# Kernel optimization log

Hardware: AMD Instinct MI355X
Metric: run time of the kernel (lower is better)

The kernel has to match this reference:

```python
import jax, jax.numpy as jnp
import numpy as np

N = 1_000_000      # occupied voxels
GRID = 256         # voxel grid extent per axis
K = 27             # 3^3 kernel offsets
CIN, COUT = 2, 16


def _build_nbr_map(coords: np.ndarray) -> np.ndarray:
    """Kernel-offset neighbor map like MinkowskiEngine's kernel map.
    coords: [N,3] unique int voxel coords. Returns [N,K] int32, -1 = no neighbor.
    """
    key = (coords[:, 0] * GRID + coords[:, 1]) * GRID + coords[:, 2]
    order = np.argsort(key)
    skey = key[order]
    offsets = np.array([[dx, dy, dz]
                        for dx in (-1, 0, 1)
                        for dy in (-1, 0, 1)
                        for dz in (-1, 0, 1)], dtype=np.int64)
    nbr = np.full((coords.shape[0], K), -1, dtype=np.int32)
    for k in range(K):
        nc = coords + offsets[k]
        valid = np.all((nc >= 0) & (nc < GRID), axis=1)
        nkey = (nc[:, 0] * GRID + nc[:, 1]) * GRID + nc[:, 2]
        pos = np.clip(np.searchsorted(skey, nkey), 0, coords.shape[0] - 1)
        hit = valid & (skey[pos] == nkey)
        nbr[:, k] = np.where(hit, order[pos].astype(np.int32), -1)
    return nbr


def setup_inputs() -> dict:
    rng = np.random.default_rng(0)
    lin = rng.choice(GRID ** 3, size=N, replace=False)  # unique voxel ids
    coords = np.stack([lin // (GRID * GRID), (lin // GRID) % GRID, lin % GRID],
                      axis=1).astype(np.int64)
    nbr = _build_nbr_map(coords)
    key = jax.random.key(0)
    k1, k2 = jax.random.split(key)
    features = jax.random.normal(k1, (N, CIN), dtype=jnp.float32)
    # MinkowskiConvolution kernel: one [Cin,Cout] matrix per kernel offset, no bias
    kernel = jax.random.normal(k2, (K, CIN, COUT), dtype=jnp.float32) * 0.1
    return {"features": features, "kernel": kernel, "nbr_idx": jnp.asarray(nbr)}


def reference(features, kernel, nbr_idx):
    # gather-GEMM-scatter sparse conv: out[n] = sum_k W_k^T x[nbr(n,k)]
    mask = (nbr_idx >= 0)
    safe = jnp.maximum(nbr_idx, 0)
    gathered = features[safe]                              # [N,K,Cin]
    gathered = gathered * mask[..., None].astype(features.dtype)
    return jnp.einsum('nkc,kcd->nd', gathered, kernel)     # [N,Cout]
```

## Files before the change

### kernel.cpp

```cpp
#include <hip/hip_runtime.h>

#define K_OFF 27
#define CIN   2
#define COUT  16
#define BLK   256
#define WPB   4
#define IPW   (64 * K_OFF)
#define NB    8

typedef __attribute__((address_space(3))) unsigned int lds_u32;
typedef __attribute__((address_space(1))) const unsigned int g_u32;

__global__ __launch_bounds__(BLK, 5) void spconv_kernel(
    const float* __restrict__ feats,
    const float* __restrict__ w,
    const int*   __restrict__ nbr,
    float*       __restrict__ out,
    int n_pts)
{
    __shared__ int    s_idx[WPB * IPW];
    __shared__ float4 s_w[8 * K_OFF];

    const int t    = threadIdx.x;
    const int lane = t & 63;
    const int wv   = t >> 6;
    const int tile = blockIdx.x * WPB + wv;
    const int p    = tile * 64 + lane;

    if (t < 8 * K_OFF) {
        const int k = t >> 3, q = t & 7;
        s_w[q * K_OFF + k] = reinterpret_cast<const float4*>(w)[t];
    }

    const bool full = ((tile + 1) * 64 <= n_pts);
    if (full) {
        const int* src = nbr + (size_t)tile * IPW;
        int*       dst = s_idx + wv * IPW;
        #pragma unroll
        for (int j = 0; j < 6; ++j) {
            __builtin_amdgcn_global_load_lds(
                (g_u32*)(src + j * 256 + lane * 4),
                (lds_u32*)(dst + j * 256), 16, 0, 0);
        }
        if (lane < 48) {
            __builtin_amdgcn_global_load_lds(
                (g_u32*)(src + 6 * 256 + lane * 4),
                (lds_u32*)(dst + 6 * 256), 16, 0, 0);
        }
    }
    __syncthreads();

    float acc[COUT];
    #pragma unroll
    for (int d = 0; d < COUT; ++d) acc[d] = 0.f;

    const float2* feats2 = reinterpret_cast<const float2*>(feats);
    const int* rowp = s_idx + wv * IPW + lane * K_OFF;

    unsigned bm = 0;
    if (full) {
        #pragma unroll
        for (int k = 0; k < K_OFF; ++k)
            bm |= (rowp[k] >= 0) ? (1u << k) : 0u;
    }

    int mx = __popc(bm);
    #pragma unroll
    for (int off = 32; off; off >>= 1) mx = max(mx, __shfl_xor(mx, off, 64));

    for (int j0 = 0; j0 < mx; j0 += NB) {
        int  kk[NB];
        bool al[NB];
        #pragma unroll
        for (int j = 0; j < NB; ++j) {
            al[j] = (bm != 0);
            kk[j] = al[j] ? (int)__builtin_ctz(bm) : 0;
            bm &= bm - 1;
        }
        int idx[NB];
        #pragma unroll
        for (int j = 0; j < NB; ++j) idx[j] = rowp[kk[j]];
        float2 f[NB];
        #pragma unroll
        for (int j = 0; j < NB; ++j) f[j] = feats2[al[j] && idx[j] > 0 ? idx[j] : 0];
        #pragma unroll
        for (int j = 0; j < NB; ++j) {
            const float fm = al[j] ? 1.0f : 0.0f;
            const float fx = f[j].x * fm, fy = f[j].y * fm;
            const int k = kk[j];
            #pragma unroll
            for (int q = 0; q < 4; ++q) {
                const float4 wa = s_w[q * K_OFF + k];
                const float4 wb = s_w[(q + 4) * K_OFF + k];
                acc[q*4+0] = fmaf(fy, wb.x, fmaf(fx, wa.x, acc[q*4+0]));
                acc[q*4+1] = fmaf(fy, wb.y, fmaf(fx, wa.y, acc[q*4+1]));
                acc[q*4+2] = fmaf(fy, wb.z, fmaf(fx, wa.z, acc[q*4+2]));
                acc[q*4+3] = fmaf(fy, wb.w, fmaf(fx, wa.w, acc[q*4+3]));
            }
        }
    }

    if (!full) {
        const bool pv = (p < n_pts);
        for (int k = 0; k < K_OFF; ++k) {
            const int idx = pv ? nbr[(size_t)p * K_OFF + k] : -1;
            const float fm = (idx >= 0) ? 1.0f : 0.0f;
            const float2 f = feats2[idx > 0 ? idx : 0];
            const float fx = f.x * fm, fy = f.y * fm;
            #pragma unroll
            for (int q = 0; q < 4; ++q) {
                const float4 wa = s_w[q * K_OFF + k];
                const float4 wb = s_w[(q + 4) * K_OFF + k];
                acc[q*4+0] = fmaf(fy, wb.x, fmaf(fx, wa.x, acc[q*4+0]));
                acc[q*4+1] = fmaf(fy, wb.y, fmaf(fx, wa.y, acc[q*4+1]));
                acc[q*4+2] = fmaf(fy, wb.z, fmaf(fx, wa.z, acc[q*4+2]));
                acc[q*4+3] = fmaf(fy, wb.w, fmaf(fx, wa.w, acc[q*4+3]));
            }
        }
    }

    if (p < n_pts) {
        float4* o = reinterpret_cast<float4*>(out + (size_t)p * COUT);
        o[0] = make_float4(acc[0],  acc[1],  acc[2],  acc[3]);
        o[1] = make_float4(acc[4],  acc[5],  acc[6],  acc[7]);
        o[2] = make_float4(acc[8],  acc[9],  acc[10], acc[11]);
        o[3] = make_float4(acc[12], acc[13], acc[14], acc[15]);
    }
}

extern "C" void kernel_launch(void* const* d_in, const int* in_sizes, int n_in,
                              void* d_out, int out_size, void* d_ws, size_t ws_size,
                              hipStream_t stream) {
    const float* feats = (const float*)d_in[0];
    const float* w     = (const float*)d_in[1];
    const int*   nbr   = (const int*)d_in[2];
    float*       out   = (float*)d_out;

    const int n_pts   = in_sizes[0] / CIN;
    const int n_tiles = (n_pts + 63) / 64;
    const int grid    = (n_tiles + WPB - 1) / WPB;

    spconv_kernel<<<grid, BLK, 0, stream>>>(feats, w, nbr, out, n_pts);
}
```

Baseline: 59.27 us.

## Make kernel persistent with double-buffered async neighbor-index staging

Turns the one-tile-per-wave kernel into a persistent grid-stride loop capped at 512 blocks. Each wave prefetches the next tile's neighbor indices into a second LDS buffer with global_load_lds while it computes the current tile. The aim is to hide index-load latency and drop per-block launch and setup overhead. In exchange, LDS use per block doubles and launch bounds drop to 2 blocks per CU, which reduces occupancy available for hiding the feature-gather latency; the gather batch also shrinks from 8 to 6.

```diff
diff --git a/kernel.cpp b/kernel.cpp
--- a/kernel.cpp
+++ b/kernel.cpp
@@ -6,125 +6,144 @@
 #define BLK   256
 #define WPB   4
 #define IPW   (64 * K_OFF)
-#define NB    8
+#define NB    6
 
 typedef __attribute__((address_space(3))) unsigned int lds_u32;
 typedef __attribute__((address_space(1))) const unsigned int g_u32;
 
-__global__ __launch_bounds__(BLK, 5) void spconv_kernel(
+__device__ __forceinline__ void stage_tile(const int* __restrict__ nbr,
+                                           int tile, int* dst, int lane) {
+    const int* src = nbr + (size_t)tile * IPW;
+    #pragma unroll
+    for (int j = 0; j < 6; ++j)
+        __builtin_amdgcn_global_load_lds((g_u32*)(src + j * 256 + lane * 4),
+                                         (lds_u32*)(dst + j * 256), 16, 0, 0);
+    if (lane < 48)
+        __builtin_amdgcn_global_load_lds((g_u32*)(src + 6 * 256 + lane * 4),
+                                         (lds_u32*)(dst + 6 * 256), 16, 0, 0);
+}
+
+__global__ __launch_bounds__(BLK, 2) void spconv_kernel(
     const float* __restrict__ feats,
     const float* __restrict__ w,
     const int*   __restrict__ nbr,
     float*       __restrict__ out,
-    int n_pts)
+    int n_pts, int n_tiles)
 {
-    __shared__ int    s_idx[WPB * IPW];
+    __shared__ int    s_idx[WPB * 2 * IPW];
     __shared__ float4 s_w[8 * K_OFF];
 
     const int t    = threadIdx.x;
     const int lane = t & 63;
     const int wv   = t >> 6;
-    const int tile = blockIdx.x * WPB + wv;
-    const int p    = tile * 64 + lane;
 
     if (t < 8 * K_OFF) {
         const int k = t >> 3, q = t & 7;
         s_w[q * K_OFF + k] = reinterpret_cast<const float4*>(w)[t];
     }
-
-    const bool full = ((tile + 1) * 64 <= n_pts);
-    if (full) {
-        const int* src = nbr + (size_t)tile * IPW;
-        int*       dst = s_idx + wv * IPW;
-        #pragma unroll
-        for (int j = 0; j < 6; ++j) {
-            __builtin_amdgcn_global_load_lds(
-                (g_u32*)(src + j * 256 + lane * 4),
-                (lds_u32*)(dst + j * 256), 16, 0, 0);
-        }
-        if (lane < 48) {
-            __builtin_amdgcn_global_load_lds(
-                (g_u32*)(src + 6 * 256 + lane * 4),
-                (lds_u32*)(dst + 6 * 256), 16, 0, 0);
-        }
-    }
     __syncthreads();
 
-    float acc[COUT];
-    #pragma unroll
-    for (int d = 0; d < COUT; ++d) acc[d] = 0.f;
+    const int n_waves = gridDim.x * WPB;
+    int* bufA = s_idx + wv * (2 * IPW);
+    int* bufB = bufA + IPW;
 
     const float2* feats2 = reinterpret_cast<const float2*>(feats);
-    const int* rowp = s_idx + wv * IPW + lane * K_OFF;
 
-    unsigned bm = 0;
-    if (full) {
+    int tile = blockIdx.x * WPB + wv;
+    if (tile >= n_tiles) return;
+
+    if ((tile + 1) * 64 <= n_pts) stage_tile(nbr, tile, bufA, lane);
+    int cur = 0;
+
+    while (true) {
+        asm volatile("s_waitcnt vmcnt(0)" ::: "memory");
+        __builtin_amdgcn_sched_barrier(0);
+        __builtin_amdgcn_wave_barrier();
+
+        const int nxt = tile + n_waves;
+        if (nxt < n_tiles && (nxt + 1) * 64 <= n_pts)
+            stage_tile(nbr, nxt, cur ? bufA : bufB, lane);
+
+        int* buf = cur ? bufB : bufA;
+        const bool tfull = ((tile + 1) * 64 <= n_pts);
+
+        float acc[COUT];
         #pragma unroll
-        for (int k = 0; k < K_OFF; ++k)
-            bm |= (rowp[k] >= 0) ? (1u << k) : 0u;
-    }
+        for (int d = 0; d < COUT; ++d) acc[d] = 0.f;
 
-    int mx = __popc(bm);
-    #pragma unroll
-    for (int off = 32; off; off >>= 1) mx = max(mx, __shfl_xor(mx, off, 64));
+        if (tfull) {
+            const int* rowp = buf + lane * K_OFF;
+            unsigned bm = 0;
+            #pragma unroll
+            for (int k = 0; k < K_OFF; ++k)
+                bm |= (rowp[k] >= 0) ? (1u << k) : 0u;
+            int mx = __popc(bm);
+            #pragma unroll
+            for (int off = 32; off; off >>= 1) mx = max(mx, __shfl_xor(mx, off, 64));
 
-    for (int j0 = 0; j0 < mx; j0 += NB) {
-        int  kk[NB];
-        bool al[NB];
-        #pragma unroll
-        for (int j = 0; j < NB; ++j) {
-            al[j] = (bm != 0);
-            kk[j] = al[j] ? (int)__builtin_ctz(bm) : 0;
-            bm &= bm - 1;
-        }
-        int idx[NB];
-        #pragma unroll
-        for (int j = 0; j < NB; ++j) idx[j] = rowp[kk[j]];
-        float2 f[NB];
-        #pragma unroll
-        for (int j = 0; j < NB; ++j) f[j] = feats2[al[j] && idx[j] > 0 ? idx[j] : 0];
-        #pragma unroll
-        for (int j = 0; j < NB; ++j) {
-            const float fm = al[j] ? 1.0f : 0.0f;
-            const float fx = f[j].x * fm, fy = f[j].y * fm;
-            const int k = kk[j];
-            #pragma unroll
-            for (int q = 0; q < 4; ++q) {
-                const float4 wa = s_w[q * K_OFF + k];
-                const float4 wb = s_w[(q + 4) * K_OFF + k];
-                acc[q*4+0] = fmaf(fy, wb.x, fmaf(fx, wa.x, acc[q*4+0]));
-                acc[q*4+1] = fmaf(fy, wb.y, fmaf(fx, wa.y, acc[q*4+1]));
-                acc[q*4+2] = fmaf(fy, wb.z, fmaf(fx, wa.z, acc[q*4+2]));
-                acc[q*4+3] = fmaf(fy, wb.w, fmaf(fx, wa.w, acc[q*4+3]));
+            for (int j0 = 0; j0 < mx; j0 += NB) {
+                int   kk[NB]; float fm[NB];
+                #pragma unroll
+                for (int j = 0; j < NB; ++j) {
+                    const bool alive = (bm != 0);
+                    kk[j] = alive ? (int)__builtin_ctz(bm) : 0;
+                    fm[j] = alive ? 1.0f : 0.0f;
+                    bm &= bm - 1;
+                }
+                int idx[NB];
+                #pragma unroll
+                for (int j = 0; j < NB; ++j) idx[j] = rowp[kk[j]];
+                float2 f[NB];
+                #pragma unroll
+                for (int j = 0; j < NB; ++j)
+                    f[j] = feats2[(fm[j] > 0.f && idx[j] > 0) ? idx[j] : 0];
+                #pragma unroll
+                for (int j = 0; j < NB; ++j) {
+                    const float fx = f[j].x * fm[j], fy = f[j].y * fm[j];
+                    const int k = kk[j];
+                    #pragma unroll
+                    for (int q = 0; q < 4; ++q) {
+                        const float4 wa = s_w[q * K_OFF + k];
+                        const float4 wb = s_w[(q + 4) * K_OFF + k];
+                        acc[q*4+0] = fmaf(fy, wb.x, fmaf(fx, wa.x, acc[q*4+0]));
+                        acc[q*4+1] = fmaf(fy, wb.y, fmaf(fx, wa.y, acc[q*4+1]));
+                        acc[q*4+2] = fmaf(fy, wb.z, fmaf(fx, wa.z, acc[q*4+2]));
+                        acc[q*4+3] = fmaf(fy, wb.w, fmaf(fx, wa.w, acc[q*4+3]));
+                    }
+                }
+            }
+        } else {
+            const int p = tile * 64 + lane;
+            const bool pv = (p < n_pts);
+            for (int k = 0; k < K_OFF; ++k) {
+                const int idx = pv ? nbr[(size_t)p * K_OFF + k] : -1;
+                const float m = (idx >= 0) ? 1.0f : 0.0f;
+                const float2 f = feats2[idx > 0 ? idx : 0];
+                const float fx = f.x * m, fy = f.y * m;
+                #pragma unroll
+                for (int q = 0; q < 4; ++q) {
+                    const float4 wa = s_w[q * K_OFF + k];
+                    const float4 wb = s_w[(q + 4) * K_OFF + k];
+                    acc[q*4+0] = fmaf(fy, wb.x, fmaf(fx, wa.x, acc[q*4+0]));
+                    acc[q*4+1] = fmaf(fy, wb.y, fmaf(fx, wa.y, acc[q*4+1]));
+                    acc[q*4+2] = fmaf(fy, wb.z, fmaf(fx, wa.z, acc[q*4+2]));
+                    acc[q*4+3] = fmaf(fy, wb.w, fmaf(fx, wa.w, acc[q*4+3]));
+                }
             }
         }
-    }
 
-    if (!full) {
-        const bool pv = (p < n_pts);
-        for (int k = 0; k < K_OFF; ++k) {
-            const int idx = pv ? nbr[(size_t)p * K_OFF + k] : -1;
-            const float fm = (idx >= 0) ? 1.0f : 0.0f;
-            const float2 f = feats2[idx > 0 ? idx : 0];
-            const float fx = f.x * fm, fy = f.y * fm;
-            #pragma unroll
-            for (int q = 0; q < 4; ++q) {
-                const float4 wa = s_w[q * K_OFF + k];
-                const float4 wb = s_w[(q + 4) * K_OFF + k];
-                acc[q*4+0] = fmaf(fy, wb.x, fmaf(fx, wa.x, acc[q*4+0]));
-                acc[q*4+1] = fmaf(fy, wb.y, fmaf(fx, wa.y, acc[q*4+1]));
-                acc[q*4+2] = fmaf(fy, wb.z, fmaf(fx, wa.z, acc[q*4+2]));
-                acc[q*4+3] = fmaf(fy, wb.w, fmaf(fx, wa.w, acc[q*4+3]));
-            }
+        const int p = tile * 64 + lane;
+        if (p < n_pts) {
+            float4* o = reinterpret_cast<float4*>(out + (size_t)p * COUT);
+            o[0] = make_float4(acc[0],  acc[1],  acc[2],  acc[3]);
+            o[1] = make_float4(acc[4],  acc[5],  acc[6],  acc[7]);
+            o[2] = make_float4(acc[8],  acc[9],  acc[10], acc[11]);
+            o[3] = make_float4(acc[12], acc[13], acc[14], acc[15]);
         }
-    }
 
-    if (p < n_pts) {
-        float4* o = reinterpret_cast<float4*>(out + (size_t)p * COUT);
-        o[0] = make_float4(acc[0],  acc[1],  acc[2],  acc[3]);
-        o[1] = make_float4(acc[4],  acc[5],  acc[6],  acc[7]);
-        o[2] = make_float4(acc[8],  acc[9],  acc[10], acc[11]);
-        o[3] = make_float4(acc[12], acc[13], acc[14], acc[15]);
+        if (nxt >= n_tiles) break;
+        tile = nxt;
+        cur ^= 1;
     }
 }
 
@@ -138,7 +157,8 @@
 
     const int n_pts   = in_sizes[0] / CIN;
     const int n_tiles = (n_pts + 63) / 64;
-    const int grid    = (n_tiles + WPB - 1) / WPB;
+    int grid = (n_tiles + WPB - 1) / WPB;
+    if (grid > 512) grid = 512;
 
-    spconv_kernel<<<grid, BLK, 0, stream>>>(feats, w, nbr, out, n_pts);
+    spconv_kernel<<<grid, BLK, 0, stream>>>(feats, w, nbr, out, n_pts, n_tiles);
 }
```

Measured after the change: 55.76 us. -5.9%, faster.
